# Optimization experiments

Hardware: AMD Instinct MI355X
Metric: run time of the kernel (lower is better)

Reference implementation:

```python
import jax, jax.numpy as jnp
import numpy as np

HIDDEN = 2048
N_HEADS = 32
N_KV = 8
HEAD_DIM = 128
EPS = 1e-6
THETA = 10000.0
WINDOW = 512
T = 2048


def _rms_norm(x, w, eps=EPS):
    # x: [..., d]
    var = jnp.mean(x * x, axis=-1, keepdims=True)
    return x * jax.lax.rsqrt(var + eps) * w


def _rope(x, positions):
    # neox-style full rotary, x: [T, H, d]
    d = x.shape[-1]
    inv_freq = 1.0 / (THETA ** (jnp.arange(0, d, 2, dtype=jnp.float32) / d))  # [d/2]
    ang = positions.astype(jnp.float32)[:, None] * inv_freq  # [T, d/2]
    cos = jnp.cos(ang)[:, None, :]  # [T,1,d/2]
    sin = jnp.sin(ang)[:, None, :]
    x1, x2 = x[..., : d // 2], x[..., d // 2 :]
    return jnp.concatenate([x1 * cos - x2 * sin, x2 * cos + x1 * sin], axis=-1)


def setup_inputs() -> dict:
    key = jax.random.key(0)
    ks = jax.random.split(key, 6)
    q_size = N_HEADS * HEAD_DIM
    kv_size = N_KV * HEAD_DIM
    s = 1.0 / np.sqrt(HIDDEN)
    return {
        "positions": jnp.arange(T, dtype=jnp.int32),
        "hidden_states": jax.random.normal(ks[0], (T, HIDDEN), dtype=jnp.float32),
        "w_qkv": jax.random.normal(ks[1], (HIDDEN, q_size + 2 * kv_size), dtype=jnp.float32) * s,
        "w_o": jax.random.normal(ks[2], (q_size, HIDDEN), dtype=jnp.float32) * s,
        "w_g": jax.random.normal(ks[3], (HIDDEN, N_HEADS), dtype=jnp.float32) * s,
        "q_norm_w": jnp.ones((HEAD_DIM,), dtype=jnp.float32),
        "k_norm_w": jnp.ones((HEAD_DIM,), dtype=jnp.float32),
    }


def reference(positions, hidden_states, w_qkv, w_o, w_g, q_norm_w, k_norm_w):
    t = hidden_states.shape[0]
    q_size = N_HEADS * HEAD_DIM
    kv_size = N_KV * HEAD_DIM
    scale = HEAD_DIM ** -0.5
    group = N_HEADS // N_KV

    qkv = hidden_states @ w_qkv  # [T, q+2kv]
    q = qkv[:, :q_size].reshape(t, N_HEADS, HEAD_DIM)
    k = qkv[:, q_size : q_size + kv_size].reshape(t, N_KV, HEAD_DIM)
    v = qkv[:, q_size + kv_size :].reshape(t, N_KV, HEAD_DIM)

    # per-head RMSNorm then RoPE
    q = _rope(_rms_norm(q, q_norm_w), positions)
    k = _rope(_rms_norm(k, k_norm_w), positions)

    # sliding-window causal attention with GQA (group queries per kv head)
    qg = q.reshape(t, N_KV, group, HEAD_DIM)
    scores = jnp.einsum("tkgd,skd->kgts", qg, k) * scale  # [Hkv,G,T,T]
    diff = positions[:, None] - positions[None, :]  # i - j
    mask = (diff >= 0) & (diff < WINDOW)  # causal + sliding window
    scores = jnp.where(mask[None, None], scores, -jnp.inf)
    probs = jax.nn.softmax(scores, axis=-1)
    attn = jnp.einsum("kgts,skd->tkgd", probs, v).reshape(t, N_HEADS, HEAD_DIM)

    # softplus gate per head, then output projection
    gate = jax.nn.softplus((hidden_states @ w_g).astype(jnp.float32)).astype(attn.dtype)
    attn = attn * gate[:, :, None]
    return attn.reshape(t, q_size) @ w_o
```

## Files before the change

### kernel.cpp

```cpp
#include <hip/hip_runtime.h>

typedef __attribute__((ext_vector_type(4))) float floatx4;
typedef __attribute__((ext_vector_type(8))) _Float16 half8;
typedef __attribute__((ext_vector_type(4))) _Float16 half4;

#define TT 2048
#define HIDDEN 2048
#define NH 32
#define NKV 8
#define HD 128
#define QSIZE 4096
#define KVSIZE 1024
#define QKVN 6144
#define QKVNP 6272
#define WQR 6400
#define VOFF 5120
#define GOFF 6144
#define WINDOW 512

__global__ __launch_bounds__(256) void prep_kernel(
    const float* __restrict__ w_qkv, const float* __restrict__ w_o,
    const float* __restrict__ hidden, const float* __restrict__ w_g,
    _Float16* __restrict__ Wqkvt, _Float16* __restrict__ Wot,
    _Float16* __restrict__ Xb) {
  __shared__ float tile[64][68];
  int bid = blockIdx.x;
  int tid = threadIdx.x;
  if (bid >= 5120) {
    if (bid < 7168) {
      int i = ((bid - 5120) * 256 + tid) * 8;
      float4 a = *(const float4*)&hidden[i];
      float4 b = *(const float4*)&hidden[i + 4];
      alignas(16) _Float16 o[8] = {(_Float16)a.x, (_Float16)a.y, (_Float16)a.z, (_Float16)a.w,
                                   (_Float16)b.x, (_Float16)b.y, (_Float16)b.z, (_Float16)b.w};
      *(uint4*)&Xb[i] = *(const uint4*)o;
    } else if (bid < 7392) {
      int i = ((bid - 7168) * 256 + tid) * 8;
      *(uint4*)&Wqkvt[(size_t)(GOFF + NH) * HIDDEN + i] = (uint4){0, 0, 0, 0};
    } else {
      int br = (bid - 7392) * 32;
      int c = tid & 31, r0 = tid >> 5;
      __shared__ float gt[32][33];
#pragma unroll
      for (int i = 0; i < 4; ++i) {
        int r = r0 + 8 * i;
        gt[r][c] = w_g[(size_t)(br + r) * NH + c];
      }
      __syncthreads();
#pragma unroll
      for (int i = 0; i < 4; ++i) {
        int r = r0 + 8 * i;
        Wqkvt[(size_t)(GOFF + r) * HIDDEN + br + c] = (_Float16)gt[c][r];
      }
    }
    return;
  }
  const float* in;
  _Float16* out;
  int R, C, tilesX, t;
  if (bid < 3072) { in = w_qkv; out = Wqkvt; R = HIDDEN; C = QKVN; tilesX = 96; t = bid; }
  else           { in = w_o;   out = Wot;   R = QSIZE;  C = HIDDEN; tilesX = 32; t = bid - 3072; }
  int bc = (t % tilesX) * 64, br = (t / tilesX) * 64;
  int rr = tid >> 4, l16 = tid & 15;
#pragma unroll
  for (int it = 0; it < 4; ++it) {
    int r = rr + it * 16;
    *(float4*)&tile[r][l16 * 4] = *(const float4*)&in[(size_t)(br + r) * C + bc + l16 * 4];
  }
  __syncthreads();
  int orow = tid >> 2, rr0 = (tid & 3) * 16;
  alignas(16) _Float16 tmp[16];
#pragma unroll
  for (int jj = 0; jj < 16; ++jj) tmp[jj] = (_Float16)tile[rr0 + jj][orow];
  *(uint4*)&out[(size_t)(bc + orow) * R + br + rr0] = *(const uint4*)&tmp[0];
  *(uint4*)&out[(size_t)(bc + orow) * R + br + rr0 + 8] = *(const uint4*)&tmp[8];
}

__global__ __launch_bounds__(256) void repack_kv_kernel(const _Float16* __restrict__ Kh,
                                                        const _Float16* __restrict__ QKVh,
                                                        _Float16* __restrict__ Kf,
                                                        _Float16* __restrict__ Vf) {
  __shared__ _Float16 tile[64][136];
  int st = blockIdx.x, kh = blockIdx.y;
  int s0 = st * 64;
  if (blockIdx.z == 0) {
    _Float16* dst = Kf + (size_t)(kh * 32 + st) * 8192;
#pragma unroll
    for (int i = 0; i < 4; ++i) {
      int c = threadIdx.x + i * 256;
      int jt = c >> 8, kc = (c >> 6) & 3, quad = (c >> 4) & 3, n16 = c & 15;
      uint4 v = *(const uint4*)&Kh[((size_t)(s0 + jt * 16 + n16) * NKV + kh) * HD +
                                   kc * 32 + quad * 8];
      *(uint4*)&dst[c * 8] = v;
    }
  } else {
#pragma unroll
    for (int i = 0; i < 4; ++i) {
      int c = threadIdx.x + i * 256;
      int row = c >> 4, part = c & 15;
      *(uint4*)&tile[row][part * 8] =
          *(const uint4*)&QKVh[(size_t)(s0 + row) * QKVNP + VOFF + kh * HD + part * 8];
    }
    __syncthreads();
    _Float16* dst = Vf + (size_t)(kh * 32 + st) * 8192;
#pragma unroll
    for (int i = 0; i < 4; ++i) {
      int c = threadIdx.x + i * 256;
      int jd = c >> 7, kc = (c >> 6) & 1, quad = (c >> 4) & 3, n16 = c & 15;
      int d = jd * 16 + n16, sb = kc * 32 + quad * 8;
      alignas(16) _Float16 tmp[8];
#pragma unroll
      for (int j = 0; j < 8; ++j) tmp[j] = tile[sb + j][d];
      *(uint4*)&dst[c * 8] = *(const uint4*)tmp;
    }
  }
}

__device__ __forceinline__ void async16(const _Float16* g, _Float16* l) {
  __builtin_amdgcn_global_load_lds((const __attribute__((address_space(1))) void*)g,
                                   (__attribute__((address_space(3))) void*)l, 16, 0, 0);
}

#define G256_K 2048

#define STG_A(ob, mh, kt)                                                        \
  async16(As0 + (size_t)(mh) * 64 * G256_K + (kt), &lds[(ob) + ((mh) * 64 + r0A0) * 64]); \
  async16(As1 + (size_t)(mh) * 64 * G256_K + (kt), &lds[(ob) + ((mh) * 64 + r0A1) * 64]);
#define STG_B(ob, nh, kt)                                                        \
  async16(Bs0 + (size_t)(nh) * 32 * G256_K + (kt), &lds[(ob) + 16384 + ((nh) * 32 + r0B0) * 64]); \
  async16(Bs1 + (size_t)(nh) * 32 * G256_K + (kt), &lds[(ob) + 16384 + ((nh) * 32 + r0B1) * 64]);

#define LD_A(mh)                                                                 \
  _Pragma("unroll") for (int fm = 0; fm < 4; ++fm)                               \
  _Pragma("unroll") for (int ks = 0; ks < 2; ++ks)                               \
    aA[fm][ks] = *(const half8*)&LA[(wm * 128 + (mh) * 64 + fm * 16 + lr) * 64 + \
                                    (((ks * 4 + quad) ^ l7) * 8)];
#define LD_B(DST, nh)                                                            \
  _Pragma("unroll") for (int fn = 0; fn < 2; ++fn)                               \
  _Pragma("unroll") for (int ks = 0; ks < 2; ++ks)                               \
    DST[fn][ks] = *(const half8*)&LB[(wn * 64 + (nh) * 32 + fn * 16 + lr) * 64 + \
                                     (((ks * 4 + quad) ^ l7) * 8)];
#define MFMAQ(BS, mh, nh)                                                        \
  __builtin_amdgcn_s_setprio(1);                                                 \
  _Pragma("unroll") for (int fm = 0; fm < 4; ++fm)                               \
  _Pragma("unroll") for (int fn = 0; fn < 2; ++fn)                               \
  _Pragma("unroll") for (int ks = 0; ks < 2; ++ks)                               \
    acc[(mh) * 4 + fm][(nh) * 2 + fn] = __builtin_amdgcn_mfma_f32_16x16x32_f16(  \
        aA[fm][ks], BS[fn][ks], acc[(mh) * 4 + fm][(nh) * 2 + fn], 0, 0, 0);     \
  __builtin_amdgcn_s_setprio(0);
#define VMW4 asm volatile("s_waitcnt vmcnt(4)" ::: "memory")
#define VMW2 asm volatile("s_waitcnt vmcnt(2)" ::: "memory")
#define VMW0 asm volatile("s_waitcnt vmcnt(0)" ::: "memory")
#define BAR __builtin_amdgcn_s_barrier()
#define SB0 __builtin_amdgcn_sched_barrier(0)

__global__ __launch_bounds__(512, 2) void gemm256_kernel(
    const _Float16* __restrict__ A, const _Float16* __restrict__ Bt,
    _Float16* __restrict__ C) {
  __shared__ _Float16 lds[65536];
  int tid = threadIdx.x;
  int wave = tid >> 6, lane = tid & 63;
  int wm = wave >> 2, wn = wave & 3;
  int lr = lane & 15, quad = lane >> 4, l7 = lane & 7, l3 = lane >> 3;
  int m0 = blockIdx.x * 256, n0 = blockIdx.y * 256;

  int q0 = wave * 2, q1 = q0 + 1;
  int r0A0 = (q0 >> 3) * 128 + (q0 & 7) * 8;
  int r0A1 = (q1 >> 3) * 128 + (q1 & 7) * 8;
  int r0B0 = (q0 >> 2) * 64 + (q0 & 3) * 8;
  int r0B1 = (q1 >> 2) * 64 + (q1 & 3) * 8;
  int gA8 = (l7 ^ l3) * 8;

  const _Float16* As0 = A + (size_t)(m0 + r0A0 + l3) * G256_K + gA8;
  const _Float16* As1 = A + (size_t)(m0 + r0A1 + l3) * G256_K + gA8;
  const _Float16* Bs0 = Bt + (size_t)(n0 + r0B0 + l3) * G256_K + gA8;
  const _Float16* Bs1 = Bt + (size_t)(n0 + r0B1 + l3) * G256_K + gA8;

  floatx4 acc[8][4];
#pragma unroll
  for (int i = 0; i < 8; ++i)
#pragma unroll
    for (int j = 0; j < 4; ++j) acc[i][j] = (floatx4){0.f, 0.f, 0.f, 0.f};

  STG_A(0, 0, 0);
  STG_B(0, 0, 0);
  STG_B(0, 1, 0);
  STG_A(0, 1, 0);
  VMW4;
  BAR;
  SB0;

  half8 aA[4][2], b0[2][2], b1[2][2];

  for (int t = 0; t < 32; ++t) {
    int bb = (t & 1) << 15;
    int ob = bb ^ 32768;
    int ktn = (t + 1) * 64;
    bool stg = (t < 31);
    const _Float16* LA = &lds[bb];
    const _Float16* LB = &lds[bb + 16384];

    LD_A(0);
    LD_B(b0, 0);
    if (stg) { STG_A(ob, 0, ktn); }
    BAR;
    MFMAQ(b0, 0, 0);
    if (stg) VMW4; else VMW2;
    BAR;
    SB0;

    LD_B(b1, 1);
    if (stg) { STG_B(ob, 0, ktn); }
    BAR;
    MFMAQ(b1, 0, 1);
    if (stg) VMW4; else VMW0;
    BAR;
    SB0;

    LD_A(1);
    if (stg) { STG_B(ob, 1, ktn); }
    BAR;
    MFMAQ(b0, 1, 0);
    BAR;
    SB0;

    if (stg) { STG_A(ob, 1, ktn); }
    BAR;
    MFMAQ(b1, 1, 1);
    if (stg) VMW4;
    BAR;
    SB0;
  }

#pragma unroll
  for (int mh = 0; mh < 2; ++mh)
#pragma unroll
    for (int fm = 0; fm < 4; ++fm)
#pragma unroll
      for (int nh = 0; nh < 2; ++nh)
#pragma unroll
        for (int fn = 0; fn < 2; ++fn)
#pragma unroll
          for (int rr = 0; rr < 4; ++rr) {
            int row = m0 + wm * 128 + mh * 64 + fm * 16 + quad * 4 + rr;
            int col = n0 + wn * 64 + nh * 32 + fn * 16 + lr;
            if (col < QKVNP)
              C[(size_t)row * QKVNP + col] = (_Float16)acc[mh * 4 + fm][nh * 2 + fn][rr];
          }
}

__device__ __forceinline__ void swizzle_mn(int& m0, int& n0) {
  int ntiles = gridDim.y;
  int pid = blockIdx.x + blockIdx.y * gridDim.x;
  int band = pid / (8 * ntiles);
  int wi = pid - band * (8 * ntiles);
  m0 = (band * 8 + (wi & 7)) * 128;
  n0 = (wi >> 3) * 128;
}

__global__ __launch_bounds__(256, 2) void gemm_bt_splitk_kernel(
    const _Float16* __restrict__ A, const _Float16* __restrict__ Bt,
    float* __restrict__ Cp, int M, int N, int K, int Ks) {
  __shared__ _Float16 As[128 * 64];
  __shared__ _Float16 Bs[128 * 64];
  int tid = threadIdx.x;
  int wave = tid >> 6, lane = tid & 63;
  int wm = wave >> 1, wn = wave & 1;
  int m0, n0;
  swizzle_mn(m0, n0);
  int kb = blockIdx.z * Ks;
  float* C = Cp + (size_t)blockIdx.z * M * N;
  int lr = lane & 15;
  int quad = lane >> 4;
  floatx4 acc[4][4];
#pragma unroll
  for (int i = 0; i < 4; ++i)
#pragma unroll
    for (int j = 0; j < 4; ++j) acc[i][j] = (floatx4){0.f, 0.f, 0.f, 0.f};

  for (int k0 = kb; k0 < kb + Ks; k0 += 64) {
    __syncthreads();
#pragma unroll
    for (int it = 0; it < 4; ++it) {
      int c = tid + it * 256;
      int row = c >> 3, j = c & 7;
      int jj = j ^ (row & 7);
      _Float16* la = &As[it * 2048 + wave * 512];
      _Float16* lb = &Bs[it * 2048 + wave * 512];
      async16(&A[(size_t)(m0 + row) * K + k0 + jj * 8], la);
      async16(&Bt[(size_t)(n0 + row) * K + k0 + jj * 8], lb);
    }
    __syncthreads();
#pragma unroll
    for (int kc = 0; kc < 2; ++kc) {
      int ch = kc * 4 + quad;
      half8 a[4], b[4];
#pragma unroll
      for (int i = 0; i < 4; ++i) {
        int r = wm * 64 + i * 16 + lr;
        a[i] = *(const half8*)&As[r * 64 + (ch ^ (r & 7)) * 8];
      }
#pragma unroll
      for (int j = 0; j < 4; ++j) {
        int r = wn * 64 + j * 16 + lr;
        b[j] = *(const half8*)&Bs[r * 64 + (ch ^ (r & 7)) * 8];
      }
#pragma unroll
      for (int i = 0; i < 4; ++i)
#pragma unroll
        for (int j = 0; j < 4; ++j)
          acc[i][j] = __builtin_amdgcn_mfma_f32_16x16x32_f16(a[i], b[j], acc[i][j], 0, 0, 0);
    }
  }
  int rq = quad * 4;
#pragma unroll
  for (int i = 0; i < 4; ++i)
#pragma unroll
    for (int j = 0; j < 4; ++j)
#pragma unroll
      for (int r = 0; r < 4; ++r) {
        int row = m0 + wm * 64 + i * 16 + rq + r;
        int col = n0 + wn * 64 + j * 16 + lr;
        C[(size_t)row * N + col] = acc[i][j][r];
      }
}

__global__ __launch_bounds__(256) void reduce2_kernel(const float* __restrict__ P,
                                                      float* __restrict__ out) {
  size_t i = ((size_t)blockIdx.x * 256 + threadIdx.x) * 8;
  const float* Q = P + (size_t)TT * HIDDEN;
  float4 a0 = *(const float4*)&P[i];
  float4 a1 = *(const float4*)&P[i + 4];
  float4 b0 = *(const float4*)&Q[i];
  float4 b1 = *(const float4*)&Q[i + 4];
  a0.x += b0.x; a0.y += b0.y; a0.z += b0.z; a0.w += b0.w;
  a1.x += b1.x; a1.y += b1.y; a1.z += b1.z; a1.w += b1.w;
  *(float4*)&out[i] = a0;
  *(float4*)&out[i + 4] = a1;
}

__global__ __launch_bounds__(256) void normrope_kernel(
    const _Float16* __restrict__ qkv, const float* __restrict__ qw,
    const float* __restrict__ kw, const int* __restrict__ positions,
    _Float16* __restrict__ qh, _Float16* __restrict__ khb) {
  int wid = blockIdx.x * 4 + (threadIdx.x >> 6);
  int lane = threadIdx.x & 63;
  int t, hh;
  const _Float16* src;
  _Float16* dst;
  const float* w;
  if (wid < TT * NH) {
    t = wid >> 5; hh = wid & 31;
    src = qkv + (size_t)t * QKVNP + hh * HD;
    dst = qh + ((size_t)t * NH + hh) * HD;
    w = qw;
  } else {
    int r = wid - TT * NH;
    t = r >> 3; hh = r & 7;
    src = qkv + (size_t)t * QKVNP + QSIZE + hh * HD;
    dst = khb + ((size_t)t * NKV + hh) * HD;
    w = kw;
  }
  float x1 = (float)src[lane];
  float x2 = (float)src[lane + 64];
  float ss = x1 * x1 + x2 * x2;
#pragma unroll
  for (int off = 1; off < 64; off <<= 1) ss += __shfl_xor(ss, off);
  float rr = rsqrtf(ss * (1.0f / 128.0f) + 1e-6f);
  float n1 = x1 * rr * w[lane];
  float n2 = x2 * rr * w[lane + 64];
  float pos = (float)positions[t];
  float invf = exp2f(-(float)lane * (13.287712379549449f / 64.0f));
  float ang = pos * invf;
  float sn, cs;
  sincosf(ang, &sn, &cs);
  dst[lane] = (_Float16)(n1 * cs - n2 * sn);
  dst[lane + 64] = (_Float16)(n2 * cs + n1 * sn);
}

#define PSTR 68
#define M0 8.0f
__global__ __launch_bounds__(256, 2) void attn_kernel(
    const _Float16* __restrict__ Qh, const _Float16* __restrict__ Kf,
    const _Float16* __restrict__ Vf, const _Float16* __restrict__ QKVh,
    _Float16* __restrict__ Og) {
  const float scale = 0.08838834764831845f;
  __shared__ _Float16 Ps[4][16 * PSTR];
  int tid = threadIdx.x;
  int wave = tid >> 6, lane = tid & 63;
  int n16 = lane & 15, quad = lane >> 4;
  int t0 = blockIdx.x * 16;
  int kh = blockIdx.y;
  int h = kh * 4 + wave;
  _Float16* ps = Ps[wave];

  half8 qf[4];
#pragma unroll
  for (int kc = 0; kc < 4; ++kc)
    qf[kc] = *(const half8*)&Qh[((size_t)(t0 + n16) * NH + h) * HD + kc * 32 + quad * 8];

  floatx4 O[8];
  float lp[4];
#pragma unroll
  for (int jd = 0; jd < 8; ++jd) O[jd] = (floatx4){0.f, 0.f, 0.f, 0.f};
#pragma unroll
  for (int r = 0; r < 4; ++r) lp[r] = 0.f;

  int lo = t0 - (WINDOW - 1);
  if (lo < 0) lo = 0;
  int st0 = lo >> 6;
  int st1 = t0 >> 6;

  half8 kfr[4][4];
  {
    const _Float16* kb = Kf + (size_t)(kh * 32 + st0) * 8192;
#pragma unroll
    for (int jt = 0; jt < 4; ++jt)
#pragma unroll
      for (int kc = 0; kc < 4; ++kc)
        kfr[jt][kc] = *(const half8*)&kb[(jt * 4 + kc) * 512 + lane * 8];
  }

  for (int st = st0; st <= st1; ++st) {
    int s0 = st * 64;
    const _Float16* vb = Vf + (size_t)(kh * 32 + st) * 8192;
    floatx4 S[4];
#pragma unroll
    for (int jt = 0; jt < 4; ++jt) S[jt] = (floatx4){0.f, 0.f, 0.f, 0.f};
#pragma unroll
    for (int jt = 0; jt < 4; ++jt)
#pragma unroll
      for (int kc = 0; kc < 4; ++kc)
        S[jt] = __builtin_amdgcn_mfma_f32_16x16x32_f16(qf[kc], kfr[jt][kc], S[jt], 0, 0, 0);
    if (st < st1) {
      const _Float16* kb = Kf + (size_t)(kh * 32 + st + 1) * 8192;
#pragma unroll
      for (int jt = 0; jt < 4; ++jt)
#pragma unroll
        for (int kc = 0; kc < 4; ++kc)
          kfr[jt][kc] = *(const half8*)&kb[(jt * 4 + kc) * 512 + lane * 8];
    }
    bool interior = (t0 >= s0 + 63) && (t0 + 15 - s0 < WINDOW);
    if (interior) {
#pragma unroll
      for (int r = 0; r < 4; ++r) {
        float rs = 0.f;
#pragma unroll
        for (int jt = 0; jt < 4; ++jt) {
          float p = __expf(__builtin_fmaf(S[jt][r], scale, -M0));
          rs += p;
          ps[(quad * 4 + r) * PSTR + jt * 16 + n16] = (_Float16)p;
        }
        lp[r] += rs;
      }
    } else {
#pragma unroll
      for (int r = 0; r < 4; ++r) {
        int tq = t0 + quad * 4 + r;
        float rs = 0.f;
#pragma unroll
        for (int jt = 0; jt < 4; ++jt) {
          int diff = tq - (s0 + jt * 16 + n16);
          bool ok = (diff >= 0) && (diff < WINDOW);
          float p = ok ? __expf(__builtin_fmaf(S[jt][r], scale, -M0)) : 0.f;
          rs += p;
          ps[(quad * 4 + r) * PSTR + jt * 16 + n16] = (_Float16)p;
        }
        lp[r] += rs;
      }
    }
    half8 pf[2];
#pragma unroll
    for (int kc = 0; kc < 2; ++kc) {
      half4 lo4 = *(const half4*)&ps[n16 * PSTR + kc * 32 + quad * 8];
      half4 hi4 = *(const half4*)&ps[n16 * PSTR + kc * 32 + quad * 8 + 4];
      pf[kc] = (half8){lo4[0], lo4[1], lo4[2], lo4[3], hi4[0], hi4[1], hi4[2], hi4[3]};
    }
#pragma unroll
    for (int jd = 0; jd < 8; ++jd) {
#pragma unroll
      for (int kc = 0; kc < 2; ++kc) {
        half8 vfr = *(const half8*)&vb[(jd * 2 + kc) * 512 + lane * 8];
        O[jd] = __builtin_amdgcn_mfma_f32_16x16x32_f16(pf[kc], vfr, O[jd], 0, 0, 0);
      }
    }
  }
#pragma unroll
  for (int r = 0; r < 4; ++r) {
    float l = lp[r];
#pragma unroll
    for (int off = 1; off < 16; off <<= 1) l += __shfl_xor(l, off);
    int t = t0 + quad * 4 + r;
    float gl = (float)QKVh[(size_t)t * QKVNP + GOFF + h];
    float g = (gl > 0.f) ? gl + log1pf(__expf(-gl)) : log1pf(__expf(gl));
    float inv = g / l;
#pragma unroll
    for (int jd = 0; jd < 8; ++jd)
      Og[(size_t)t * QSIZE + h * HD + jd * 16 + n16] = (_Float16)(O[jd][r] * inv);
  }
}

extern "C" void kernel_launch(void* const* d_in, const int* in_sizes, int n_in,
                              void* d_out, int out_size, void* d_ws, size_t ws_size,
                              hipStream_t stream) {
  const int* positions = (const int*)d_in[0];
  const float* hidden = (const float*)d_in[1];
  const float* w_qkv = (const float*)d_in[2];
  const float* w_o = (const float*)d_in[3];
  const float* w_g = (const float*)d_in[4];
  const float* q_norm_w = (const float*)d_in[5];
  const float* k_norm_w = (const float*)d_in[6];
  float* out = (float*)d_out;

  char* ws = (char*)d_ws;
  size_t off = 0;
  auto alloc = [&](size_t bytes) {
    void* p = ws + off;
    off += (bytes + 255) & ~(size_t)255;
    return p;
  };
  _Float16* Xb = (_Float16*)alloc((size_t)TT * HIDDEN * 2);
  _Float16* Wqkvt = (_Float16*)alloc((size_t)WQR * HIDDEN * 2);
  _Float16* Wot = (_Float16*)alloc((size_t)HIDDEN * QSIZE * 2);
  _Float16* QKVh = (_Float16*)alloc((size_t)TT * QKVNP * 2);
  _Float16* Qh = (_Float16*)alloc((size_t)TT * NH * HD * 2);
  _Float16* Kh = (_Float16*)alloc((size_t)TT * NKV * HD * 2);
  _Float16* Kf = (_Float16*)alloc((size_t)NKV * 32 * 8192 * 2);
  _Float16* Vf = (_Float16*)alloc((size_t)NKV * 32 * 8192 * 2);
  _Float16* Og = (_Float16*)alloc((size_t)TT * QSIZE * 2);
  float* Cp = (float*)ws;

  prep_kernel<<<7456, 256, 0, stream>>>(w_qkv, w_o, hidden, w_g, Wqkvt, Wot, Xb);
  gemm256_kernel<<<dim3(TT / 256, WQR / 256), 512, 0, stream>>>(Xb, Wqkvt, QKVh);
  normrope_kernel<<<(TT * (NH + NKV)) / 4, 256, 0, stream>>>(QKVh, q_norm_w, k_norm_w,
                                                             positions, Qh, Kh);
  repack_kv_kernel<<<dim3(32, NKV, 2), 256, 0, stream>>>(Kh, QKVh, Kf, Vf);
  attn_kernel<<<dim3(TT / 16, NKV), 256, 0, stream>>>(Qh, Kf, Vf, QKVh, Og);
  gemm_bt_splitk_kernel<<<dim3(TT / 128, HIDDEN / 128, 2), 256, 0, stream>>>(
      Og, Wot, Cp, TT, HIDDEN, QSIZE, QSIZE / 2);
  reduce2_kernel<<<(TT * HIDDEN) / (256 * 8), 256, 0, stream>>>(Cp, out);
}
```

Before: 315.6 us.

## Simplify GEMM main loop to issue all prefetches upfront with one barrier

Restructures the 256x256 GEMM k-loop: all async global-to-LDS loads for the next tile are issued at the start of each iteration, then all fragments are read from LDS and the MFMAs run without intermediate barriers. A single vmcnt(0) wait and barrier close each iteration, and a second A-fragment register set lets the scheduler interleave freely. This drops three of the four barriers per iteration, at the cost of more registers and a full drain of memory loads before each barrier.

```diff
diff --git a/kernel.cpp b/kernel.cpp
--- a/kernel.cpp
+++ b/kernel.cpp
@@ -130,26 +130,24 @@
   async16(Bs0 + (size_t)(nh) * 32 * G256_K + (kt), &lds[(ob) + 16384 + ((nh) * 32 + r0B0) * 64]); \
   async16(Bs1 + (size_t)(nh) * 32 * G256_K + (kt), &lds[(ob) + 16384 + ((nh) * 32 + r0B1) * 64]);
 
-#define LD_A(mh)                                                                 \
+#define LD_A(DST, mh)                                                            \
   _Pragma("unroll") for (int fm = 0; fm < 4; ++fm)                               \
   _Pragma("unroll") for (int ks = 0; ks < 2; ++ks)                               \
-    aA[fm][ks] = *(const half8*)&LA[(wm * 128 + (mh) * 64 + fm * 16 + lr) * 64 + \
-                                    (((ks * 4 + quad) ^ l7) * 8)];
+    DST[fm][ks] = *(const half8*)&LA[(wm * 128 + (mh) * 64 + fm * 16 + lr) * 64 + \
+                                     (((ks * 4 + quad) ^ l7) * 8)];
 #define LD_B(DST, nh)                                                            \
   _Pragma("unroll") for (int fn = 0; fn < 2; ++fn)                               \
   _Pragma("unroll") for (int ks = 0; ks < 2; ++ks)                               \
     DST[fn][ks] = *(const half8*)&LB[(wn * 64 + (nh) * 32 + fn * 16 + lr) * 64 + \
                                      (((ks * 4 + quad) ^ l7) * 8)];
-#define MFMAQ(BS, mh, nh)                                                        \
+#define MFMAQ(AS, BS, mh, nh)                                                    \
   __builtin_amdgcn_s_setprio(1);                                                 \
   _Pragma("unroll") for (int fm = 0; fm < 4; ++fm)                               \
   _Pragma("unroll") for (int fn = 0; fn < 2; ++fn)                               \
   _Pragma("unroll") for (int ks = 0; ks < 2; ++ks)                               \
     acc[(mh) * 4 + fm][(nh) * 2 + fn] = __builtin_amdgcn_mfma_f32_16x16x32_f16(  \
-        aA[fm][ks], BS[fn][ks], acc[(mh) * 4 + fm][(nh) * 2 + fn], 0, 0, 0);     \
+        AS[fm][ks], BS[fn][ks], acc[(mh) * 4 + fm][(nh) * 2 + fn], 0, 0, 0);     \
   __builtin_amdgcn_s_setprio(0);
-#define VMW4 asm volatile("s_waitcnt vmcnt(4)" ::: "memory")
-#define VMW2 asm volatile("s_waitcnt vmcnt(2)" ::: "memory")
 #define VMW0 asm volatile("s_waitcnt vmcnt(0)" ::: "memory")
 #define BAR __builtin_amdgcn_s_barrier()
 #define SB0 __builtin_amdgcn_sched_barrier(0)
@@ -183,14 +181,14 @@
     for (int j = 0; j < 4; ++j) acc[i][j] = (floatx4){0.f, 0.f, 0.f, 0.f};
 
   STG_A(0, 0, 0);
+  STG_A(0, 1, 0);
   STG_B(0, 0, 0);
   STG_B(0, 1, 0);
-  STG_A(0, 1, 0);
-  VMW4;
+  VMW0;
   BAR;
   SB0;
 
-  half8 aA[4][2], b0[2][2], b1[2][2];
+  half8 a0f[4][2], a1f[4][2], b0[2][2], b1[2][2];
 
   for (int t = 0; t < 32; ++t) {
     int bb = (t & 1) << 15;
@@ -200,34 +198,23 @@
     const _Float16* LA = &lds[bb];
     const _Float16* LB = &lds[bb + 16384];
 
-    LD_A(0);
+    if (stg) {
+      STG_A(ob, 0, ktn);
+      STG_B(ob, 0, ktn);
+      STG_B(ob, 1, ktn);
+      STG_A(ob, 1, ktn);
+    }
+
     LD_B(b0, 0);
-    if (stg) { STG_A(ob, 0, ktn); }
-    BAR;
-    MFMAQ(b0, 0, 0);
-    if (stg) VMW4; else VMW2;
-    BAR;
-    SB0;
-
+    LD_A(a0f, 0);
+    MFMAQ(a0f, b0, 0, 0);
     LD_B(b1, 1);
-    if (stg) { STG_B(ob, 0, ktn); }
-    BAR;
-    MFMAQ(b1, 0, 1);
-    if (stg) VMW4; else VMW0;
-    BAR;
-    SB0;
-
-    LD_A(1);
-    if (stg) { STG_B(ob, 1, ktn); }
-    BAR;
-    MFMAQ(b0, 1, 0);
-    BAR;
-    SB0;
-
-    if (stg) { STG_A(ob, 1, ktn); }
-    BAR;
-    MFMAQ(b1, 1, 1);
-    if (stg) VMW4;
+    MFMAQ(a0f, b1, 0, 1);
+    LD_A(a1f, 1);
+    MFMAQ(a1f, b0, 1, 0);
+    MFMAQ(a1f, b1, 1, 1);
+
+    if (stg) VMW0;
     BAR;
     SB0;
   }
```

Measured after the change: 315.4 us. No clear change (-0.1%).

## Deepen QKV GEMM prefetch pipeline and remap block order for L2 locality

Applied to the files above, without the earlier changes.

Restructures the 256x256 QKV GEMM main loop so global-to-LDS staging runs up to two k-steps ahead, reusing the current buffer's freed halves, and adds explicit lgkmcnt waits before the MFMAs. The staging layout changes to contiguous per-wave 16-row slabs. The launch becomes a 1D grid of 200 blocks with a remap that groups blocks sharing A and B tiles, aiming for better L2 reuse. This risks LDS write-after-read hazards in the deeper pipeline and more waitcnt stalls.

```diff
diff --git a/kernel.cpp b/kernel.cpp
--- a/kernel.cpp
+++ b/kernel.cpp
@@ -123,19 +123,19 @@
 
 #define G256_K 2048
 
-#define STG_A(ob, mh, kt)                                                        \
-  async16(As0 + (size_t)(mh) * 64 * G256_K + (kt), &lds[(ob) + ((mh) * 64 + r0A0) * 64]); \
-  async16(As1 + (size_t)(mh) * 64 * G256_K + (kt), &lds[(ob) + ((mh) * 64 + r0A1) * 64]);
-#define STG_B(ob, nh, kt)                                                        \
-  async16(Bs0 + (size_t)(nh) * 32 * G256_K + (kt), &lds[(ob) + 16384 + ((nh) * 32 + r0B0) * 64]); \
-  async16(Bs1 + (size_t)(nh) * 32 * G256_K + (kt), &lds[(ob) + 16384 + ((nh) * 32 + r0B1) * 64]);
-
-#define LD_A(mh)                                                                 \
+#define STG_A(fb, h, kt)                                                         \
+  async16(pA0 + (size_t)(h) * 128 * G256_K + (kt) * 64, &lds[(fb) + (h) * 8192 + wave * 1024]); \
+  async16(pA1 + (size_t)(h) * 128 * G256_K + (kt) * 64, &lds[(fb) + (h) * 8192 + wave * 1024 + 512]);
+#define STG_B(fb, h, kt)                                                         \
+  async16(pB0 + (size_t)(h) * 128 * G256_K + (kt) * 64, &lds[(fb) + 16384 + (h) * 8192 + wave * 1024]); \
+  async16(pB1 + (size_t)(h) * 128 * G256_K + (kt) * 64, &lds[(fb) + 16384 + (h) * 8192 + wave * 1024 + 512]);
+
+#define LDA(mh)                                                                  \
   _Pragma("unroll") for (int fm = 0; fm < 4; ++fm)                               \
   _Pragma("unroll") for (int ks = 0; ks < 2; ++ks)                               \
-    aA[fm][ks] = *(const half8*)&LA[(wm * 128 + (mh) * 64 + fm * 16 + lr) * 64 + \
-                                    (((ks * 4 + quad) ^ l7) * 8)];
-#define LD_B(DST, nh)                                                            \
+    a[fm][ks] = *(const half8*)&LA[(wm * 128 + (mh) * 64 + fm * 16 + lr) * 64 +  \
+                                   (((ks * 4 + quad) ^ l7) * 8)];
+#define LDB(DST, nh)                                                             \
   _Pragma("unroll") for (int fn = 0; fn < 2; ++fn)                               \
   _Pragma("unroll") for (int ks = 0; ks < 2; ++ks)                               \
     DST[fn][ks] = *(const half8*)&LB[(wn * 64 + (nh) * 32 + fn * 16 + lr) * 64 + \
@@ -146,11 +146,10 @@
   _Pragma("unroll") for (int fn = 0; fn < 2; ++fn)                               \
   _Pragma("unroll") for (int ks = 0; ks < 2; ++ks)                               \
     acc[(mh) * 4 + fm][(nh) * 2 + fn] = __builtin_amdgcn_mfma_f32_16x16x32_f16(  \
-        aA[fm][ks], BS[fn][ks], acc[(mh) * 4 + fm][(nh) * 2 + fn], 0, 0, 0);     \
+        a[fm][ks], BS[fn][ks], acc[(mh) * 4 + fm][(nh) * 2 + fn], 0, 0, 0);      \
   __builtin_amdgcn_s_setprio(0);
-#define VMW4 asm volatile("s_waitcnt vmcnt(4)" ::: "memory")
-#define VMW2 asm volatile("s_waitcnt vmcnt(2)" ::: "memory")
-#define VMW0 asm volatile("s_waitcnt vmcnt(0)" ::: "memory")
+#define VMW(n) asm volatile("s_waitcnt vmcnt(" #n ")" ::: "memory")
+#define LGKM0 asm volatile("s_waitcnt lgkmcnt(0)" ::: "memory")
 #define BAR __builtin_amdgcn_s_barrier()
 #define SB0 __builtin_amdgcn_sched_barrier(0)
 
@@ -162,19 +161,16 @@
   int wave = tid >> 6, lane = tid & 63;
   int wm = wave >> 2, wn = wave & 3;
   int lr = lane & 15, quad = lane >> 4, l7 = lane & 7, l3 = lane >> 3;
-  int m0 = blockIdx.x * 256, n0 = blockIdx.y * 256;
-
-  int q0 = wave * 2, q1 = q0 + 1;
-  int r0A0 = (q0 >> 3) * 128 + (q0 & 7) * 8;
-  int r0A1 = (q1 >> 3) * 128 + (q1 & 7) * 8;
-  int r0B0 = (q0 >> 2) * 64 + (q0 & 3) * 8;
-  int r0B1 = (q1 >> 2) * 64 + (q1 & 3) * 8;
-  int gA8 = (l7 ^ l3) * 8;
-
-  const _Float16* As0 = A + (size_t)(m0 + r0A0 + l3) * G256_K + gA8;
-  const _Float16* As1 = A + (size_t)(m0 + r0A1 + l3) * G256_K + gA8;
-  const _Float16* Bs0 = Bt + (size_t)(n0 + r0B0 + l3) * G256_K + gA8;
-  const _Float16* Bs1 = Bt + (size_t)(n0 + r0B1 + l3) * G256_K + gA8;
+
+  int bid = blockIdx.x;
+  int o = (bid & 7) * 25 + (bid >> 3);
+  int m0 = (o & 7) * 256, n0 = (o >> 3) * 256;
+
+  int gsw = (l7 ^ l3) * 8;
+  const _Float16* pA0 = A + (size_t)(m0 + wave * 16 + l3) * G256_K + gsw;
+  const _Float16* pA1 = A + (size_t)(m0 + wave * 16 + 8 + l3) * G256_K + gsw;
+  const _Float16* pB0 = Bt + (size_t)(n0 + wave * 16 + l3) * G256_K + gsw;
+  const _Float16* pB1 = Bt + (size_t)(n0 + wave * 16 + 8 + l3) * G256_K + gsw;
 
   floatx4 acc[8][4];
 #pragma unroll
@@ -182,71 +178,74 @@
 #pragma unroll
     for (int j = 0; j < 4; ++j) acc[i][j] = (floatx4){0.f, 0.f, 0.f, 0.f};
 
+  STG_B(0, 0, 0);
   STG_A(0, 0, 0);
-  STG_B(0, 0, 0);
+  STG_A(0, 1, 0);
   STG_B(0, 1, 0);
-  STG_A(0, 1, 0);
-  VMW4;
+  STG_B(32768, 0, 1);
+  STG_A(32768, 0, 1);
+  VMW(4);
   BAR;
   SB0;
 
-  half8 aA[4][2], b0[2][2], b1[2][2];
-
-  for (int t = 0; t < 32; ++t) {
-    int bb = (t & 1) << 15;
-    int ob = bb ^ 32768;
-    int ktn = (t + 1) * 64;
-    bool stg = (t < 31);
-    const _Float16* LA = &lds[bb];
-    const _Float16* LB = &lds[bb + 16384];
-
-    LD_A(0);
-    LD_B(b0, 0);
-    if (stg) { STG_A(ob, 0, ktn); }
-    BAR;
+  half8 a[4][2], b0[2][2], b1[2][2];
+
+  for (int S = 0; S < 32; ++S) {
+    int cb = (S & 1) << 15;
+    int nb = cb ^ 32768;
+    const _Float16* LA = &lds[cb];
+    const _Float16* LB = &lds[cb + 16384];
+    bool s1 = (S + 1) < 32, s2 = (S + 2) < 32;
+
+    LDA(0);
+    LDB(b0, 0);
+    if (s1) { STG_A(nb, 1, S + 1); }
+    BAR;
+    LGKM0;
+    SB0;
     MFMAQ(b0, 0, 0);
-    if (stg) VMW4; else VMW2;
-    BAR;
-    SB0;
-
-    LD_B(b1, 1);
-    if (stg) { STG_B(ob, 0, ktn); }
-    BAR;
+    BAR;
+    SB0;
+
+    LDB(b1, 1);
+    if (s1) { STG_B(nb, 1, S + 1); }
+    BAR;
+    LGKM0;
+    SB0;
     MFMAQ(b1, 0, 1);
-    if (stg) VMW4; else VMW0;
-    BAR;
-    SB0;
-
-    LD_A(1);
-    if (stg) { STG_B(ob, 1, ktn); }
-    BAR;
+    BAR;
+    SB0;
+
+    LDA(1);
+    if (s2) { STG_B(cb, 0, S + 2); }
+    BAR;
+    LGKM0;
+    SB0;
     MFMAQ(b0, 1, 0);
     BAR;
     SB0;
 
-    if (stg) { STG_A(ob, 1, ktn); }
-    BAR;
+    if (s2) { STG_A(cb, 0, S + 2); }
+    BAR;
+    SB0;
     MFMAQ(b1, 1, 1);
-    if (stg) VMW4;
-    BAR;
-    SB0;
-  }
-
-#pragma unroll
-  for (int mh = 0; mh < 2; ++mh)
-#pragma unroll
-    for (int fm = 0; fm < 4; ++fm)
-#pragma unroll
-      for (int nh = 0; nh < 2; ++nh)
-#pragma unroll
-        for (int fn = 0; fn < 2; ++fn)
-#pragma unroll
-          for (int rr = 0; rr < 4; ++rr) {
-            int row = m0 + wm * 128 + mh * 64 + fm * 16 + quad * 4 + rr;
-            int col = n0 + wn * 64 + nh * 32 + fn * 16 + lr;
-            if (col < QKVNP)
-              C[(size_t)row * QKVNP + col] = (_Float16)acc[mh * 4 + fm][nh * 2 + fn][rr];
-          }
+    if (S < 30) VMW(4);
+    else if (S == 30) VMW(0);
+    BAR;
+    SB0;
+  }
+
+#pragma unroll
+  for (int i = 0; i < 8; ++i)
+#pragma unroll
+    for (int j = 0; j < 4; ++j)
+#pragma unroll
+      for (int rr = 0; rr < 4; ++rr) {
+        int row = m0 + wm * 128 + i * 16 + quad * 4 + rr;
+        int col = n0 + wn * 64 + j * 16 + lr;
+        if (col < QKVNP)
+          C[(size_t)row * QKVNP + col] = (_Float16)acc[i][j][rr];
+      }
 }
 
 __device__ __forceinline__ void swizzle_mn(int& m0, int& n0) {
@@ -531,7 +530,7 @@
   float* Cp = (float*)ws;
 
   prep_kernel<<<7456, 256, 0, stream>>>(w_qkv, w_o, hidden, w_g, Wqkvt, Wot, Xb);
-  gemm256_kernel<<<dim3(TT / 256, WQR / 256), 512, 0, stream>>>(Xb, Wqkvt, QKVh);
+  gemm256_kernel<<<200, 512, 0, stream>>>(Xb, Wqkvt, QKVh);
   normrope_kernel<<<(TT * (NH + NKV)) / 4, 256, 0, stream>>>(QKVh, q_norm_w, k_norm_w,
                                                              positions, Qh, Kh);
   repack_kv_kernel<<<dim3(32, NKV, 2), 256, 0, stream>>>(Kh, QKVh, Kf, Vf);
```

New measurement: 314.2 us. About the same (-0.4%).
